# Kernel optimization log

Hardware: AMD Instinct MI355X
Metric: run time of the kernel (lower is better)

Reference implementation:

```python
import jax, jax.numpy as jnp
import numpy as np

H = 1024
N_IDX = 400000
NBINS = 256


def setup_inputs() -> dict:
    key = jax.random.key(0)
    ks = jax.random.split(key, 10)
    return {
        "input_data": jax.random.uniform(ks[0], (1, 3, H, H), jnp.float32),
        "target_data": jax.random.uniform(ks[1], (1, 3, H, H), jnp.float32) * 2.0 - 1.0,
        "ref": jax.random.uniform(ks[2], (1, 3, H, H), jnp.float32) * 2.0 - 1.0,
        "mask_src": (jax.random.uniform(ks[3], (1, 1, H, H)) > 0.3).astype(jnp.float32) * 255.0,
        "mask_tar": (jax.random.uniform(ks[4], (1, 1, H, H)) > 0.3).astype(jnp.float32) * 255.0,
        "target_data_eye": jax.random.uniform(ks[5], (1, 3, H, H), jnp.float32),
        "idx0": jax.random.randint(ks[6], (N_IDX,), 0, H),
        "idx1": jax.random.randint(ks[7], (N_IDX,), 0, H),
        "idx2": jax.random.randint(ks[8], (N_IDX,), 0, H),
        "idx3": jax.random.randint(ks[9], (N_IDX,), 0, H),
    }


def _cdf(vals):
    # vals: [3, N] float in [0, 256). torch.histc(bins=256, min=0, max=256) -> bin = floor(v)
    bins = jnp.clip(vals.astype(jnp.int32), 0, NBINS - 1)  # [3, N]
    hist = jnp.zeros((3, NBINS), jnp.float32).at[jnp.arange(3)[:, None], bins].add(1.0)
    cdf = jnp.cumsum(hist, axis=1)
    return cdf / cdf[:, -1:]  # normalized cumulative histogram, [3, 256]


def _trans_table(cdf_dst, cdf_ref):
    # cal_trans(ref=cdf_dst, adj=cdf_ref): table[i] = first j in [1,255]
    # with cdf_ref[j-1] <= cdf_dst[i] <= cdf_ref[j]; else table[i] = i; table[255] = 255
    r = cdf_dst[:, None]                  # [256, 1]
    lo = cdf_ref[None, :-1]               # [1, 255] -> adj[j-1], j = 1..255
    hi = cdf_ref[None, 1:]                # [1, 255] -> adj[j]
    cond = (r >= lo) & (r <= hi)          # [256, 255]
    has = cond.any(axis=1)
    j = jnp.argmax(cond, axis=1) + 1      # first matching j
    table = jnp.where(has, j, jnp.arange(NBINS))
    return table.at[NBINS - 1].set(NBINS - 1)


def _hist_match(dst_img, ref_img, i0, i1, i2, i3):
    # dst_img, ref_img: [3, H, W]; gather masked pixels per channel
    dst_align = dst_img[:, i0, i1]        # [3, N]
    ref_align = ref_img[:, i2, i3]        # [3, N]
    cdf_dst = _cdf(dst_align)
    cdf_ref = _cdf(ref_align)
    tables = jax.vmap(_trans_table)(cdf_dst, cdf_ref)  # [3, 256] int
    bins = jnp.clip(dst_align.astype(jnp.int32), 0, NBINS - 1)  # int() truncation, v >= 0
    matched = jnp.take_along_axis(tables, bins, axis=1).astype(dst_img.dtype)  # [3, N]
    return dst_img.at[:, i0, i1].set(matched)


def reference(input_data, target_data, ref, mask_src, mask_tar, target_data_eye,
              idx0, idx1, idx2, idx3):
    # part = 'lip' (generic part) -> histogram_matching branch; use_vgg = False
    de_norm = lambda x: jnp.clip((x + 1.0) / 2.0, 0.0, 1.0)
    target = (de_norm(target_data) * 255.0)[0]          # [3, H, W]
    inp = (jnp.clip(input_data, 0.0, 1.0) * 255.0)[0]   # [3, H, W]
    r = (de_norm(ref) * 255.0)[0]                       # [3, H, W]
    msrc = jnp.broadcast_to(mask_src / 255.0, (1, 3, H, H))[0]
    mtar = jnp.broadcast_to(mask_tar / 255.0, (1, 3, H, H))[0]

    input_masked = inp * msrc
    target_masked = target * mtar
    ref_masked = r * msrc

    input_match = jax.lax.stop_gradient(
        _hist_match(ref_masked, target_masked, idx0, idx1, idx2, idx3))

    loss = jnp.mean(jnp.abs(input_masked / 255.0 - input_match / 255.0))
    return ((target_masked / 255.0)[None], (ref_masked / 255.0)[None],
            (input_masked / 255.0)[None], (input_match / 255.0)[None], loss)
```

## Files before the change

kernel.cpp:

```cpp
#include <hip/hip_runtime.h>

#define H 1024
#define HH (H * H)
#define CHW (3 * HH)
#define NB 256
#define HIST_BLOCKS 512
#define FIN_BLOCKS 512

__device__ __forceinline__ float clamp01(float x) { return fminf(fmaxf(x, 0.0f), 1.0f); }

__device__ __forceinline__ unsigned int bin8(float v01) {
    int b = (int)(v01 * 255.0f);
    return (unsigned int)min(max(b, 0), NB - 1);
}

__global__ void k_elementwise(const float4* __restrict__ inp,
                              const float4* __restrict__ tar,
                              const float4* __restrict__ rfp,
                              const float4* __restrict__ msrc,
                              const float4* __restrict__ mtar,
                              float4* __restrict__ out0, float4* __restrict__ out1,
                              float4* __restrict__ out2,
                              uint4* __restrict__ pk_dst, uint4* __restrict__ pk_ref,
                              unsigned int* __restrict__ gz,
                              unsigned int* __restrict__ bm,
                              float* __restrict__ loss)
{
    if (blockIdx.x == 0) {
        for (int i = threadIdx.x; i < 1536; i += blockDim.x) gz[i] = 0u;
        if (threadIdx.x == 0) *loss = 0.0f;
    } else if (blockIdx.x <= 32) {
        int base = (int)(blockIdx.x - 1) * 1024;
        for (int i = threadIdx.x; i < 1024; i += blockDim.x) bm[base + i] = 0u;
    }
    int p = blockIdx.x * blockDim.x + threadIdx.x;
    if (p >= HH / 4) return;
    float4 ms4 = msrc[p], mt4 = mtar[p];
    float msx = ms4.x / 255.0f, msy = ms4.y / 255.0f, msz = ms4.z / 255.0f, msw = ms4.w / 255.0f;
    float mtx = mt4.x / 255.0f, mty = mt4.y / 255.0f, mtz = mt4.z / 255.0f, mtw = mt4.w / 255.0f;
    unsigned int bd0 = 0, bd1 = 0, bd2 = 0, bd3 = 0;
    unsigned int br0 = 0, br1 = 0, br2 = 0, br3 = 0;
#pragma unroll
    for (int c = 0; c < 3; ++c) {
        int q = c * (HH / 4) + p;
        float4 t = tar[q], r = rfp[q], iv = inp[q];
        float4 o0, o1, o2;
        o0.x = clamp01((t.x + 1.0f) * 0.5f) * mtx;
        o0.y = clamp01((t.y + 1.0f) * 0.5f) * mty;
        o0.z = clamp01((t.z + 1.0f) * 0.5f) * mtz;
        o0.w = clamp01((t.w + 1.0f) * 0.5f) * mtw;
        o1.x = clamp01((r.x + 1.0f) * 0.5f) * msx;
        o1.y = clamp01((r.y + 1.0f) * 0.5f) * msy;
        o1.z = clamp01((r.z + 1.0f) * 0.5f) * msz;
        o1.w = clamp01((r.w + 1.0f) * 0.5f) * msw;
        o2.x = clamp01(iv.x) * msx;
        o2.y = clamp01(iv.y) * msy;
        o2.z = clamp01(iv.z) * msz;
        o2.w = clamp01(iv.w) * msw;
        out0[q] = o0;
        out1[q] = o1;
        out2[q] = o2;
        int sh = 8 * c;
        bd0 |= bin8(o1.x) << sh;  bd1 |= bin8(o1.y) << sh;
        bd2 |= bin8(o1.z) << sh;  bd3 |= bin8(o1.w) << sh;
        br0 |= bin8(o0.x) << sh;  br1 |= bin8(o0.y) << sh;
        br2 |= bin8(o0.z) << sh;  br3 |= bin8(o0.w) << sh;
    }
    pk_dst[p] = make_uint4(bd0, bd1, bd2, bd3);
    pk_ref[p] = make_uint4(br0, br1, br2, br3);
}

__global__ void k_hist(const unsigned int* __restrict__ pk_dst,
                       const unsigned int* __restrict__ pk_ref,
                       const int* __restrict__ i0, const int* __restrict__ i1,
                       const int* __restrict__ i2, const int* __restrict__ i3,
                       unsigned int* __restrict__ ghist,
                       unsigned int* __restrict__ bm, int n)
{
    __shared__ unsigned int h[2 * 3 * NB];
    for (int i = threadIdx.x; i < 2 * 3 * NB; i += blockDim.x) h[i] = 0u;
    __syncthreads();

    int lane = threadIdx.x & 63;
    for (int k = blockIdx.x * blockDim.x + threadIdx.x; k < n; k += gridDim.x * blockDim.x) {
        int pd = i0[k] * H + i1[k];
        int pr = i2[k] * H + i3[k];
        unsigned int a = pk_dst[pd];
        unsigned int b = pk_ref[pr];

        atomicOr(&bm[(unsigned int)pd >> 5], 1u << (pd & 31));

        unsigned long long mza = __ballot(a == 0u);
        if (a != 0u) {
            atomicAdd(&h[        (a       & 255u)], 1u);
            atomicAdd(&h[  NB + ((a >> 8) & 255u)], 1u);
            atomicAdd(&h[2*NB + ((a >>16) & 255u)], 1u);
        } else if (lane == __ffsll(mza) - 1) {
            unsigned int cnt = (unsigned int)__popcll(mza);
            atomicAdd(&h[0],      cnt);
            atomicAdd(&h[NB],     cnt);
            atomicAdd(&h[2 * NB], cnt);
        }

        unsigned long long mzb = __ballot(b == 0u);
        if (b != 0u) {
            atomicAdd(&h[3*NB + ( b       & 255u)], 1u);
            atomicAdd(&h[4*NB + ((b >> 8) & 255u)], 1u);
            atomicAdd(&h[5*NB + ((b >>16) & 255u)], 1u);
        } else if (lane == __ffsll(mzb) - 1) {
            unsigned int cnt = (unsigned int)__popcll(mzb);
            atomicAdd(&h[3 * NB], cnt);
            atomicAdd(&h[4 * NB], cnt);
            atomicAdd(&h[5 * NB], cnt);
        }
    }
    __syncthreads();
    for (int i = threadIdx.x; i < 2 * 3 * NB; i += blockDim.x) {
        unsigned int v = h[i];
        if (v) atomicAdd(&ghist[i], v);
    }
}

__global__ __launch_bounds__(384)
void k_finalize(const uint4* __restrict__ ghist4,
                const unsigned int* __restrict__ bm,
                const float4* __restrict__ out1v,
                const float4* __restrict__ out2v,
                float4* __restrict__ out3v,
                float* __restrict__ loss)
{
    __shared__ float cdf[6][NB];
    __shared__ float tl[3 * NB];
    __shared__ float ws[6];
    int t = threadIdx.x;
    int wave = t >> 6, lane = t & 63;

    uint4 v = ghist4[wave * 64 + lane];
    unsigned int s0 = v.x;
    unsigned int s1 = s0 + v.y;
    unsigned int s2 = s1 + v.z;
    unsigned int s3 = s2 + v.w;

    unsigned int scan = s3;
#pragma unroll
    for (int off = 1; off < 64; off <<= 1) {
        unsigned int u = (unsigned int)__shfl_up((int)scan, off, 64);
        if (lane >= off) scan += u;
    }
    unsigned int prefix = scan - s3;
    unsigned int total  = (unsigned int)__shfl((int)scan, 63, 64);
    float ft = (float)total;

    cdf[wave][lane * 4 + 0] = (float)(prefix + s0) / ft;
    cdf[wave][lane * 4 + 1] = (float)(prefix + s1) / ft;
    cdf[wave][lane * 4 + 2] = (float)(prefix + s2) / ft;
    cdf[wave][lane * 4 + 3] = (float)(prefix + s3) / ft;
    __syncthreads();

    if (t < NB) {
#pragma unroll
        for (int c = 0; c < 3; ++c) {
            float r = cdf[c][t];
            const float* cr = cdf[3 + c];
            int lo = 1, hi = NB - 1;
#pragma unroll
            for (int it = 0; it < 8; ++it) {
                int mid = (lo + hi) >> 1;
                if (cr[mid] >= r) hi = mid; else lo = mid + 1;
            }
            int jstar = lo - 1;
            int tab = (jstar == 0 && cr[0] > r) ? t : (jstar + 1);
            if (t == NB - 1) tab = NB - 1;
            tl[c * NB + t] = (float)tab / 255.0f;
        }
    }
    __syncthreads();

    float s = 0.0f;
    const int n4 = HH / 4;
    for (int k = blockIdx.x * blockDim.x + t; k < n4; k += gridDim.x * blockDim.x) {
        unsigned int w = bm[k >> 3];
        unsigned int nib = (w >> ((k & 7) * 4)) & 0xFu;
#pragma unroll
        for (int c = 0; c < 3; ++c) {
            float4 a = out1v[c * n4 + k];
            float4 b = out2v[c * n4 + k];
            float4 o;
            o.x = (nib & 1u) ? tl[c * NB + bin8(a.x)] : a.x;
            o.y = (nib & 2u) ? tl[c * NB + bin8(a.y)] : a.y;
            o.z = (nib & 4u) ? tl[c * NB + bin8(a.z)] : a.z;
            o.w = (nib & 8u) ? tl[c * NB + bin8(a.w)] : a.w;
            out3v[c * n4 + k] = o;
            s += fabsf(b.x - o.x) + fabsf(b.y - o.y) + fabsf(b.z - o.z) + fabsf(b.w - o.w);
        }
    }
#pragma unroll
    for (int off = 32; off > 0; off >>= 1) s += __shfl_down(s, off);
    if (lane == 0) ws[wave] = s;
    __syncthreads();
    if (t == 0) {
        float tsum = ws[0] + ws[1] + ws[2] + ws[3] + ws[4] + ws[5];
        atomicAdd(loss, tsum * (1.0f / (float)CHW));
    }
}

extern "C" void kernel_launch(void* const* d_in, const int* in_sizes, int n_in,
                              void* d_out, int out_size, void* d_ws, size_t ws_size,
                              hipStream_t stream)
{
    const float* inp  = (const float*)d_in[0];
    const float* tar  = (const float*)d_in[1];
    const float* rfp  = (const float*)d_in[2];
    const float* msrc = (const float*)d_in[3];
    const float* mtar = (const float*)d_in[4];
    const int* i0 = (const int*)d_in[6];
    const int* i1 = (const int*)d_in[7];
    const int* i2 = (const int*)d_in[8];
    const int* i3 = (const int*)d_in[9];
    int n = in_sizes[6];

    float* out0 = (float*)d_out;
    float* out1 = out0 + CHW;
    float* out2 = out1 + CHW;
    float* out3 = out2 + CHW;
    float* loss = out3 + CHW;

    unsigned int* ghist  = (unsigned int*)d_ws;
    unsigned int* bm     = (unsigned int*)((char*)d_ws + 8192);
    unsigned int* pk_dst = (unsigned int*)((char*)d_ws + 139264);
    unsigned int* pk_ref = pk_dst + HH;

    k_elementwise<<<(HH / 4 + 255) / 256, 256, 0, stream>>>(
        (const float4*)inp, (const float4*)tar, (const float4*)rfp,
        (const float4*)msrc, (const float4*)mtar,
        (float4*)out0, (float4*)out1, (float4*)out2,
        (uint4*)pk_dst, (uint4*)pk_ref, ghist, bm, loss);

    k_hist<<<HIST_BLOCKS, 512, 0, stream>>>(pk_dst, pk_ref, i0, i1, i2, i3, ghist, bm, n);

    k_finalize<<<FIN_BLOCKS, 384, 0, stream>>>(
        (const uint4*)ghist, bm, (const float4*)out1, (const float4*)out2,
        (float4*)out3, loss);
}
```

Baseline: 170.7 us.

## Fold gather-mask bit into packed bins and read them in finalize

```diff
diff --git a/kernel.cpp b/kernel.cpp
--- a/kernel.cpp
+++ b/kernel.cpp
@@ -5,7 +5,10 @@
 #define CHW (3 * HH)
 #define NB 256
 #define HIST_BLOCKS 512
-#define FIN_BLOCKS 512
+#define FIN_BLOCKS 1024
+
+#define MARK (1u << 24)
+#define BINS3 0x00FFFFFFu
 
 __device__ __forceinline__ float clamp01(float x) { return fminf(fmaxf(x, 0.0f), 1.0f); }
 
@@ -23,15 +26,11 @@
                               float4* __restrict__ out2,
                               uint4* __restrict__ pk_dst, uint4* __restrict__ pk_ref,
                               unsigned int* __restrict__ gz,
-                              unsigned int* __restrict__ bm,
                               float* __restrict__ loss)
 {
     if (blockIdx.x == 0) {
         for (int i = threadIdx.x; i < 1536; i += blockDim.x) gz[i] = 0u;
         if (threadIdx.x == 0) *loss = 0.0f;
-    } else if (blockIdx.x <= 32) {
-        int base = (int)(blockIdx.x - 1) * 1024;
-        for (int i = threadIdx.x; i < 1024; i += blockDim.x) bm[base + i] = 0u;
     }
     int p = blockIdx.x * blockDim.x + threadIdx.x;
     if (p >= HH / 4) return;
@@ -70,12 +69,11 @@
     pk_ref[p] = make_uint4(br0, br1, br2, br3);
 }
 
-__global__ void k_hist(const unsigned int* __restrict__ pk_dst,
+__global__ void k_hist(unsigned int* __restrict__ pk_dst,
                        const unsigned int* __restrict__ pk_ref,
                        const int* __restrict__ i0, const int* __restrict__ i1,
                        const int* __restrict__ i2, const int* __restrict__ i3,
-                       unsigned int* __restrict__ ghist,
-                       unsigned int* __restrict__ bm, int n)
+                       unsigned int* __restrict__ ghist, int n)
 {
     __shared__ unsigned int h[2 * 3 * NB];
     for (int i = threadIdx.x; i < 2 * 3 * NB; i += blockDim.x) h[i] = 0u;
@@ -85,10 +83,8 @@
     for (int k = blockIdx.x * blockDim.x + threadIdx.x; k < n; k += gridDim.x * blockDim.x) {
         int pd = i0[k] * H + i1[k];
         int pr = i2[k] * H + i3[k];
-        unsigned int a = pk_dst[pd];
+        unsigned int a = atomicOr(&pk_dst[pd], MARK) & BINS3;
         unsigned int b = pk_ref[pr];
-
-        atomicOr(&bm[(unsigned int)pd >> 5], 1u << (pd & 31));
 
         unsigned long long mza = __ballot(a == 0u);
         if (a != 0u) {
@@ -121,9 +117,9 @@
     }
 }
 
-__global__ __launch_bounds__(384)
+__global__ __launch_bounds__(256)
 void k_finalize(const uint4* __restrict__ ghist4,
-                const unsigned int* __restrict__ bm,
+                const uint4* __restrict__ pkv,
                 const float4* __restrict__ out1v,
                 const float4* __restrict__ out2v,
                 float4* __restrict__ out3v,
@@ -131,33 +127,32 @@
 {
     __shared__ float cdf[6][NB];
     __shared__ float tl[3 * NB];
-    __shared__ float ws[6];
+    __shared__ float ws[4];
     int t = threadIdx.x;
     int wave = t >> 6, lane = t & 63;
 
-    uint4 v = ghist4[wave * 64 + lane];
-    unsigned int s0 = v.x;
-    unsigned int s1 = s0 + v.y;
-    unsigned int s2 = s1 + v.z;
-    unsigned int s3 = s2 + v.w;
-
-    unsigned int scan = s3;
-#pragma unroll
-    for (int off = 1; off < 64; off <<= 1) {
-        unsigned int u = (unsigned int)__shfl_up((int)scan, off, 64);
-        if (lane >= off) scan += u;
-    }
-    unsigned int prefix = scan - s3;
-    unsigned int total  = (unsigned int)__shfl((int)scan, 63, 64);
-    float ft = (float)total;
-
-    cdf[wave][lane * 4 + 0] = (float)(prefix + s0) / ft;
-    cdf[wave][lane * 4 + 1] = (float)(prefix + s1) / ft;
-    cdf[wave][lane * 4 + 2] = (float)(prefix + s2) / ft;
-    cdf[wave][lane * 4 + 3] = (float)(prefix + s3) / ft;
-    __syncthreads();
-
-    if (t < NB) {
+    for (int row = wave; row < 6; row += 4) {
+        uint4 v = ghist4[row * 64 + lane];
+        unsigned int s0 = v.x;
+        unsigned int s1 = s0 + v.y;
+        unsigned int s2 = s1 + v.z;
+        unsigned int s3 = s2 + v.w;
+        unsigned int scan = s3;
+#pragma unroll
+        for (int off = 1; off < 64; off <<= 1) {
+            unsigned int u = (unsigned int)__shfl_up((int)scan, off, 64);
+            if (lane >= off) scan += u;
+        }
+        unsigned int prefix = scan - s3;
+        float ft = (float)(unsigned int)__shfl((int)scan, 63, 64);
+        cdf[row][lane * 4 + 0] = (float)(prefix + s0) / ft;
+        cdf[row][lane * 4 + 1] = (float)(prefix + s1) / ft;
+        cdf[row][lane * 4 + 2] = (float)(prefix + s2) / ft;
+        cdf[row][lane * 4 + 3] = (float)(prefix + s3) / ft;
+    }
+    __syncthreads();
+
+    {
 #pragma unroll
         for (int c = 0; c < 3; ++c) {
             float r = cdf[c][t];
@@ -176,30 +171,30 @@
     }
     __syncthreads();
 
+    const int n4 = HH / 4;
+    const int k = blockIdx.x * 256 + t;
+    uint4 pk = pkv[k];
     float s = 0.0f;
-    const int n4 = HH / 4;
-    for (int k = blockIdx.x * blockDim.x + t; k < n4; k += gridDim.x * blockDim.x) {
-        unsigned int w = bm[k >> 3];
-        unsigned int nib = (w >> ((k & 7) * 4)) & 0xFu;
-#pragma unroll
-        for (int c = 0; c < 3; ++c) {
-            float4 a = out1v[c * n4 + k];
-            float4 b = out2v[c * n4 + k];
-            float4 o;
-            o.x = (nib & 1u) ? tl[c * NB + bin8(a.x)] : a.x;
-            o.y = (nib & 2u) ? tl[c * NB + bin8(a.y)] : a.y;
-            o.z = (nib & 4u) ? tl[c * NB + bin8(a.z)] : a.z;
-            o.w = (nib & 8u) ? tl[c * NB + bin8(a.w)] : a.w;
-            out3v[c * n4 + k] = o;
-            s += fabsf(b.x - o.x) + fabsf(b.y - o.y) + fabsf(b.z - o.z) + fabsf(b.w - o.w);
-        }
+#pragma unroll
+    for (int c = 0; c < 3; ++c) {
+        const float* tc = &tl[c * NB];
+        int sh = 8 * c;
+        float4 a = out1v[c * n4 + k];
+        float4 b = out2v[c * n4 + k];
+        float4 o;
+        o.x = (pk.x & MARK) ? tc[(pk.x >> sh) & 255u] : a.x;
+        o.y = (pk.y & MARK) ? tc[(pk.y >> sh) & 255u] : a.y;
+        o.z = (pk.z & MARK) ? tc[(pk.z >> sh) & 255u] : a.z;
+        o.w = (pk.w & MARK) ? tc[(pk.w >> sh) & 255u] : a.w;
+        out3v[c * n4 + k] = o;
+        s += fabsf(b.x - o.x) + fabsf(b.y - o.y) + fabsf(b.z - o.z) + fabsf(b.w - o.w);
     }
 #pragma unroll
     for (int off = 32; off > 0; off >>= 1) s += __shfl_down(s, off);
     if (lane == 0) ws[wave] = s;
     __syncthreads();
     if (t == 0) {
-        float tsum = ws[0] + ws[1] + ws[2] + ws[3] + ws[4] + ws[5];
+        float tsum = ws[0] + ws[1] + ws[2] + ws[3];
         atomicAdd(loss, tsum * (1.0f / (float)CHW));
     }
 }
@@ -226,19 +221,18 @@
     float* loss = out3 + CHW;
 
     unsigned int* ghist  = (unsigned int*)d_ws;
-    unsigned int* bm     = (unsigned int*)((char*)d_ws + 8192);
-    unsigned int* pk_dst = (unsigned int*)((char*)d_ws + 139264);
+    unsigned int* pk_dst = (unsigned int*)((char*)d_ws + 8192);
     unsigned int* pk_ref = pk_dst + HH;
 
     k_elementwise<<<(HH / 4 + 255) / 256, 256, 0, stream>>>(
         (const float4*)inp, (const float4*)tar, (const float4*)rfp,
         (const float4*)msrc, (const float4*)mtar,
         (float4*)out0, (float4*)out1, (float4*)out2,
-        (uint4*)pk_dst, (uint4*)pk_ref, ghist, bm, loss);
-
-    k_hist<<<HIST_BLOCKS, 512, 0, stream>>>(pk_dst, pk_ref, i0, i1, i2, i3, ghist, bm, n);
-
-    k_finalize<<<FIN_BLOCKS, 384, 0, stream>>>(
-        (const uint4*)ghist, bm, (const float4*)out1, (const float4*)out2,
-        (float4*)out3, loss);
-}
+        (uint4*)pk_dst, (uint4*)pk_ref, ghist, loss);
+
+    k_hist<<<HIST_BLOCKS, 512, 0, stream>>>(pk_dst, pk_ref, i0, i1, i2, i3, ghist, n);
+
+    k_finalize<<<FIN_BLOCKS, 256, 0, stream>>>(
+        (const uint4*)ghist, (const uint4*)pk_dst,
+        (const float4*)out1, (const float4*)out2, (float4*)out3, loss);
+}
```

New measurement: 170.9 us. No clear change (+0.1%).
